# Performance work log

Measured on AMD Instinct MI355X. Metric: run time of the kernel, lower is better.

## Reference

```python
import jax, jax.numpy as jnp
import numpy as np

PRIOR = 0.2
TEMP = 1.0
THRESHOLD = 0.5
B, L, D, H = 8, 4096, 768, 512


def setup_inputs() -> dict:
    key = jax.random.key(0)
    k1, k2, k3, k4 = jax.random.split(key, 4)
    hidden = jax.random.normal(k1, (B, L, D), jnp.float32)
    # MLP params: Linear(D,H) -> ReLU -> Linear(H,1)
    W1 = jax.random.normal(k2, (D, H), jnp.float32) / np.sqrt(D).astype(np.float32)
    b1 = jnp.zeros((H,), jnp.float32)
    W2 = jax.random.normal(k3, (H, 1), jnp.float32) / np.sqrt(H).astype(np.float32)
    b2 = jnp.zeros((1,), jnp.float32)
    # pre-sampled uniform noise for the RelaxedBernoulli logistic reparameterization
    noise_u = jax.random.uniform(k4, (B, L), jnp.float32, minval=1e-6, maxval=1.0 - 1e-6)
    return dict(hidden=hidden, W1=W1, b1=b1, W2=W2, b2=b2, noise_u=noise_u)


def reference(hidden, W1, b1, W2, b2, noise_u):
    bs, seq_len, model_dim = hidden.shape
    # boundary MLP -> per-token logits [B, L]
    h = jax.nn.relu(jnp.einsum('bld,dh->blh', hidden, W1) + b1)
    logits = (jnp.einsum('blh,ho->blo', h, W2) + b2)[..., 0]
    # RelaxedBernoulli rsample: sigmoid((logits + logistic_noise) / temp),
    # since logit(sigmoid(logits)) == logits
    logistic_noise = jnp.log(noise_u) - jnp.log1p(-noise_u)
    soft_boundaries = jax.nn.sigmoid((logits + logistic_noise) / TEMP)
    hard_bin = (soft_boundaries > THRESHOLD).astype(soft_boundaries.dtype)
    # straight-through estimator
    hard_boundaries = soft_boundaries + jax.lax.stop_gradient(hard_bin - soft_boundaries)
    # segment id of each token: number of boundaries strictly before it
    # (boundary token is the last element of its segment)
    seg = (jnp.cumsum(hard_bin, axis=1) - hard_bin).astype(jnp.int32)  # [B, L] in [0, L)
    ids = (seg + seq_len * jnp.arange(bs, dtype=jnp.int32)[:, None]).reshape(-1)
    flat = hidden.reshape(bs * seq_len, model_dim)
    seg_sum = jax.ops.segment_sum(flat, ids, num_segments=bs * seq_len)
    seg_cnt = jax.ops.segment_sum(jnp.ones((bs * seq_len,), hidden.dtype), ids,
                                  num_segments=bs * seq_len)
    # mean pooling per segment; unused segment slots stay zero (padded to L segments,
    # equivalent to the torch [S,B,D]->transpose output up to zero padding)
    pooled = (seg_sum / jnp.maximum(seg_cnt, 1.0)[:, None]).reshape(bs, seq_len, model_dim)
    # hinge loss on boundary rate: penalize |rate - (prior+0.05)| beyond margin 0.05
    ratio = jnp.mean(hard_boundaries)
    loss = jax.nn.relu(jnp.abs(ratio - (PRIOR + 0.05)) - 0.05)
    num_boundaries = jnp.sum(hard_bin)
    total_positions = jnp.asarray(bs * seq_len, jnp.float32)
    return pooled, loss, num_boundaries, total_positions
```

## Files before the change

### kernel.cpp

```cpp
#include <hip/hip_runtime.h>
#include <math.h>

typedef __attribute__((ext_vector_type(8))) short short8;
typedef __attribute__((ext_vector_type(4))) float float4v;
typedef unsigned int uint;

#define BATCH 8
#define SEQ   4096
#define DIM   768
#define HID   512
#define M_TOK (BATCH * SEQ)

static __device__ __forceinline__ short f2bf_rne(float x) {
    unsigned int u = __float_as_uint(x);
    unsigned int r = (u + 0x7FFFu + ((u >> 16) & 1u)) >> 16;
    return (short)r;
}
static __device__ __forceinline__ uint pack_bf2(float a, float b) {
    return __builtin_amdgcn_perm(__float_as_uint(b), __float_as_uint(a), 0x07060302u);
}

__global__ __launch_bounds__(256) void prep_kernel(const float* __restrict__ W1,
                                                   short* __restrict__ W1T) {
    int idx = blockIdx.x * 256 + threadIdx.x;
    if (idx < DIM * HID) {
        int k = idx / HID, n = idx % HID;
        W1T[n * DIM + k] = f2bf_rne(W1[idx]);
    }
}

__global__ __launch_bounds__(256) void mlp_kernel(const float* __restrict__ A,
                                                  const short* __restrict__ BT,
                                                  const float* __restrict__ b1,
                                                  const float* __restrict__ W2,
                                                  float* __restrict__ partial) {
    __shared__ short As[128 * 40];
    __shared__ short Bs[128 * 40];

    const int id  = blockIdx.x;
    const int m_t = (id & 7) + ((id >> 5) << 3);
    const int n_t = (id >> 3) & 3;
    const int m0 = m_t << 7, n0 = n_t << 7;

    const int tid  = threadIdx.x;
    const int srow = tid >> 1;
    const int shalf = tid & 1;
    const int wave = tid >> 6, lane = tid & 63;
    const int quad = lane >> 4, r = lane & 15;
    const int waveM = (wave & 1) << 6, waveN = (wave >> 1) << 6;

    float4v acc[4][4] = {};

    const float* aRow = A + (size_t)(m0 + srow) * DIM + shalf * 16;
    const short* bRow = BT + (size_t)(n0 + srow) * DIM + shalf * 16;

    const int lw = srow * 40 + shalf * 16;
    const int la = (waveM + r) * 40 + quad * 8;
    const int lb = (waveN + r) * 40 + quad * 8;

    float4v fA[2][4];
    short8  fB[2][2];
#pragma unroll
    for (int i = 0; i < 4; i++) fA[0][i] = *(const float4v*)(aRow + i * 4);
    fB[0][0] = *(const short8*)(bRow);
    fB[0][1] = *(const short8*)(bRow + 8);

#pragma unroll
    for (int it = 0; it < 24; ++it) {
        const int cur = it & 1;
        if (it + 1 < 24) {
            const float* ap = aRow + (it + 1) * 32;
            const short* bp = bRow + (it + 1) * 32;
#pragma unroll
            for (int i = 0; i < 4; i++) fA[cur ^ 1][i] = *(const float4v*)(ap + i * 4);
            fB[cur ^ 1][0] = *(const short8*)(bp);
            fB[cur ^ 1][1] = *(const short8*)(bp + 8);
        }
        uint pk[8];
#pragma unroll
        for (int i = 0; i < 4; i++) {
            pk[2 * i]     = pack_bf2(fA[cur][i][0], fA[cur][i][1]);
            pk[2 * i + 1] = pack_bf2(fA[cur][i][2], fA[cur][i][3]);
        }
        __syncthreads();
        *(short8*)(&As[lw])     = *(short8*)&pk[0];
        *(short8*)(&As[lw + 8]) = *(short8*)&pk[4];
        *(short8*)(&Bs[lw])     = fB[cur][0];
        *(short8*)(&Bs[lw + 8]) = fB[cur][1];
        __syncthreads();

        short8 af[4], bf[4];
#pragma unroll
        for (int i = 0; i < 4; i++) {
            af[i] = *(const short8*)(&As[la + i * 16 * 40]);
            bf[i] = *(const short8*)(&Bs[lb + i * 16 * 40]);
        }
#pragma unroll
        for (int mi = 0; mi < 4; mi++)
#pragma unroll
            for (int ni = 0; ni < 4; ni++)
                acc[mi][ni] = __builtin_amdgcn_mfma_f32_16x16x32_bf16(
                    af[mi], bf[ni], acc[mi][ni], 0, 0, 0);
    }

    float w2v[4], b1v[4];
#pragma unroll
    for (int ni = 0; ni < 4; ni++) {
        int gc = n0 + waveN + ni * 16 + r;
        w2v[ni] = W2[gc];
        b1v[ni] = b1[gc];
    }
    const int buf = n_t * 2 + (waveN >> 6);
#pragma unroll
    for (int mi = 0; mi < 4; mi++) {
#pragma unroll
        for (int v = 0; v < 4; v++) {
            float p = 0.f;
#pragma unroll
            for (int ni = 0; ni < 4; ni++) {
                float h = acc[mi][ni][v] + b1v[ni];
                h = h > 0.f ? h : 0.f;
                p += h * w2v[ni];
            }
#pragma unroll
            for (int off = 1; off < 16; off <<= 1) p += __shfl_xor(p, off, 64);
            if (r == 0) {
                int gr = m0 + waveM + mi * 16 + quad * 4 + v;
                partial[(size_t)buf * M_TOK + gr] = p;
            }
        }
    }
}

__global__ __launch_bounds__(1024) void boundary_kernel(const float* __restrict__ partial,
                                                        const float* __restrict__ b2p,
                                                        const float* __restrict__ noise,
                                                        int* __restrict__ starts,
                                                        int* __restrict__ nseg,
                                                        int* __restrict__ nbcount) {
    const int b = blockIdx.x, tid = threadIdx.x;
    const int base = tid * 4;
    const float b2 = b2p[0];
    int h[4], c = 0;
#pragma unroll
    for (int j = 0; j < 4; j++) {
        int l = base + j;
        float u = noise[b * SEQ + l];
        float nz = logf(u) - log1pf(-u);
        float lg = b2 + nz;
#pragma unroll
        for (int q = 0; q < 8; q++) lg += partial[(size_t)q * M_TOK + b * SEQ + l];
        h[j] = (lg > 0.f) ? 1 : 0;
        c += h[j];
    }
    const int lane = tid & 63, wid = tid >> 6;
    int inc = c;
    for (int off = 1; off < 64; off <<= 1) {
        int t = __shfl_up(inc, off, 64);
        if (lane >= off) inc += t;
    }
    __shared__ int wtot[16], woff[16], extra[2];
    if (lane == 63) wtot[wid] = inc;
    if (tid == 1023) extra[0] = h[3];
    __syncthreads();
    if (tid == 0) {
        int s = 0;
        for (int i = 0; i < 16; i++) { woff[i] = s; s += wtot[i]; }
        extra[1] = s;
    }
    __syncthreads();
    int run = (inc - c) + woff[wid];
#pragma unroll
    for (int j = 0; j < 4; j++) {
        int l = base + j;
        if (h[j]) {
            run++;
            if (l < SEQ - 1) starts[b * (SEQ + 1) + run] = l + 1;
        }
    }
    if (tid == 0) {
        int total = extra[1];
        int ns = total + (extra[0] ? 0 : 1);
        starts[b * (SEQ + 1)] = 0;
        starts[b * (SEQ + 1) + ns] = SEQ;
        nseg[b] = ns;
        nbcount[b] = total;
    }
}

__global__ __launch_bounds__(256) void pool_kernel(const float* __restrict__ hidden,
                                                   const int* __restrict__ starts,
                                                   const int* __restrict__ nseg,
                                                   float* __restrict__ out) {
    const int wid = threadIdx.x >> 6, lane = threadIdx.x & 63;
    const int s = blockIdx.x * 4 + wid, b = blockIdx.y;
    float* orow = out + (size_t)(b * SEQ + s) * DIM;
    const int ns = nseg[b];
    if (s >= ns) {
        float4v z = {0.f, 0.f, 0.f, 0.f};
        *(float4v*)(orow + lane * 4)         = z;
        *(float4v*)(orow + (lane + 64) * 4)  = z;
        *(float4v*)(orow + (lane + 128) * 4) = z;
        return;
    }
    const int st = starts[b * (SEQ + 1) + s];
    const int en = starts[b * (SEQ + 1) + s + 1];
    float4v a0 = {0.f, 0.f, 0.f, 0.f}, a1 = a0, a2 = a0;
    const float* hbase = hidden + (size_t)(b * SEQ) * DIM;
    for (int row = st; row < en; row++) {
        const float* hr = hbase + (size_t)row * DIM;
        a0 += *(const float4v*)(hr + lane * 4);
        a1 += *(const float4v*)(hr + (lane + 64) * 4);
        a2 += *(const float4v*)(hr + (lane + 128) * 4);
    }
    const float invc = 1.f / (float)(en - st);
    a0 *= invc; a1 *= invc; a2 *= invc;
    *(float4v*)(orow + lane * 4)         = a0;
    *(float4v*)(orow + (lane + 64) * 4)  = a1;
    *(float4v*)(orow + (lane + 128) * 4) = a2;
}

__global__ void finalize_kernel(const int* __restrict__ nbcount, float* __restrict__ tail) {
    int nb = 0;
    for (int i = 0; i < BATCH; i++) nb += nbcount[i];
    float ratio = (float)nb / (float)M_TOK;
    float d = fabsf(ratio - 0.25f) - 0.05f;
    tail[0] = d > 0.f ? d : 0.f;
    tail[1] = (float)nb;
    tail[2] = (float)M_TOK;
}

extern "C" void kernel_launch(void* const* d_in, const int* in_sizes, int n_in,
                              void* d_out, int out_size, void* d_ws, size_t ws_size,
                              hipStream_t stream) {
    const float* hidden = (const float*)d_in[0];
    const float* W1     = (const float*)d_in[1];
    const float* b1     = (const float*)d_in[2];
    const float* W2     = (const float*)d_in[3];
    const float* b2     = (const float*)d_in[4];
    const float* noise  = (const float*)d_in[5];

    char* ws = (char*)d_ws;
    short* W1T     = (short*)(ws);
    float* partial = (float*)(ws + 786432);
    int*   starts  = (int*)(ws + 786432 + 1048576);
    int*   nseg    = (int*)(ws + 786432 + 1048576 + 131104);
    int*   nbcount = nseg + 8;
    float* out     = (float*)d_out;

    prep_kernel<<<1536, 256, 0, stream>>>(W1, W1T);
    mlp_kernel<<<1024, 256, 0, stream>>>(hidden, W1T, b1, W2, partial);
    boundary_kernel<<<BATCH, 1024, 0, stream>>>(partial, b2, noise, starts, nseg, nbcount);
    pool_kernel<<<dim3(SEQ / 4, BATCH), 256, 0, stream>>>(hidden, starts, nseg, out);
    finalize_kernel<<<1, 1, 0, stream>>>(nbcount, out + (size_t)M_TOK * DIM);
}
```

Baseline: 256.2 us.

## Load A fragments directly into registers and split boundary scan into parallel kernels

The MLP GEMM now has each wave load its own 16 rows of fp32 activations straight from global memory into MFMA fragment registers, converting them to bf16 there, so activations no longer pass through LDS. Only W1 is staged in shared memory, the tile becomes 64x128 with a 64-wide K step, and the grid doubles to 2048 blocks. The single-block-per-batch boundary scan is replaced by a 64-block ballot kernel that writes bitmasks and popcounts, followed by a 64-block kernel that scatters segment starts. The aim is to cut LDS traffic and barriers in the GEMM and to parallelise the serial scan, at the cost of uncoalesced A loads and an extra kernel launch.

```diff
diff --git a/kernel.cpp b/kernel.cpp
--- a/kernel.cpp
+++ b/kernel.cpp
@@ -19,6 +19,7 @@
 static __device__ __forceinline__ uint pack_bf2(float a, float b) {
     return __builtin_amdgcn_perm(__float_as_uint(b), __float_as_uint(a), 0x07060302u);
 }
+union FragU { uint u[4]; short8 s; };
 
 __global__ __launch_bounds__(256) void prep_kernel(const float* __restrict__ W1,
                                                    short* __restrict__ W1T) {
@@ -34,157 +35,154 @@
                                                   const float* __restrict__ b1,
                                                   const float* __restrict__ W2,
                                                   float* __restrict__ partial) {
-    __shared__ short As[128 * 40];
-    __shared__ short Bs[128 * 40];
-
-    const int id  = blockIdx.x;
-    const int m_t = (id & 7) + ((id >> 5) << 3);
-    const int n_t = (id >> 3) & 3;
-    const int m0 = m_t << 7, n0 = n_t << 7;
-
-    const int tid  = threadIdx.x;
-    const int srow = tid >> 1;
-    const int shalf = tid & 1;
-    const int wave = tid >> 6, lane = tid & 63;
+    __shared__ short Bs[2 * 128 * 40];
+
+    const int id   = blockIdx.x;
+    const int row8 = id & 7;
+    const int n_g  = (id >> 3) & 3;
+    const int m_t  = (id >> 5) * 8 + row8;
+    const int m0 = m_t * 64, n0 = n_g * 128;
+
+    const int tid = threadIdx.x, wave = tid >> 6, lane = tid & 63;
     const int quad = lane >> 4, r = lane & 15;
-    const int waveM = (wave & 1) << 6, waveN = (wave >> 1) << 6;
-
-    float4v acc[4][4] = {};
-
-    const float* aRow = A + (size_t)(m0 + srow) * DIM + shalf * 16;
-    const short* bRow = BT + (size_t)(n0 + srow) * DIM + shalf * 16;
-
-    const int lw = srow * 40 + shalf * 16;
-    const int la = (waveM + r) * 40 + quad * 8;
-    const int lb = (waveN + r) * 40 + quad * 8;
+
+    const float* aRow = A + (size_t)(m0 + wave * 16 + r) * DIM + quad * 8;
+    const short* bRow = BT + (size_t)(n0 + (tid >> 1)) * DIM + (tid & 1) * 32;
+    const int bwr = (tid & 1) * 5120 + (tid >> 1) * 40;
 
     float4v fA[2][4];
-    short8  fB[2][2];
-#pragma unroll
-    for (int i = 0; i < 4; i++) fA[0][i] = *(const float4v*)(aRow + i * 4);
-    fB[0][0] = *(const short8*)(bRow);
-    fB[0][1] = *(const short8*)(bRow + 8);
-
-#pragma unroll
-    for (int it = 0; it < 24; ++it) {
+    short8  fB[2][4];
+#pragma unroll
+    for (int i = 0; i < 4; i++) fB[0][i] = *(const short8*)(bRow + i * 8);
+    fA[0][0] = *(const float4v*)(aRow + 0);
+    fA[0][1] = *(const float4v*)(aRow + 4);
+    fA[0][2] = *(const float4v*)(aRow + 32);
+    fA[0][3] = *(const float4v*)(aRow + 36);
+
+    float4v acc[8] = {};
+
+#pragma unroll
+    for (int it = 0; it < 12; ++it) {
         const int cur = it & 1;
-        if (it + 1 < 24) {
-            const float* ap = aRow + (it + 1) * 32;
-            const short* bp = bRow + (it + 1) * 32;
-#pragma unroll
-            for (int i = 0; i < 4; i++) fA[cur ^ 1][i] = *(const float4v*)(ap + i * 4);
-            fB[cur ^ 1][0] = *(const short8*)(bp);
-            fB[cur ^ 1][1] = *(const short8*)(bp + 8);
-        }
-        uint pk[8];
-#pragma unroll
-        for (int i = 0; i < 4; i++) {
-            pk[2 * i]     = pack_bf2(fA[cur][i][0], fA[cur][i][1]);
-            pk[2 * i + 1] = pack_bf2(fA[cur][i][2], fA[cur][i][3]);
+        if (it < 11) {
+            const float* ap = aRow + (it + 1) * 64;
+            fA[cur ^ 1][0] = *(const float4v*)(ap + 0);
+            fA[cur ^ 1][1] = *(const float4v*)(ap + 4);
+            fA[cur ^ 1][2] = *(const float4v*)(ap + 32);
+            fA[cur ^ 1][3] = *(const float4v*)(ap + 36);
+            const short* bp = bRow + (it + 1) * 64;
+#pragma unroll
+            for (int i = 0; i < 4; i++) fB[cur ^ 1][i] = *(const short8*)(bp + i * 8);
         }
         __syncthreads();
-        *(short8*)(&As[lw])     = *(short8*)&pk[0];
-        *(short8*)(&As[lw + 8]) = *(short8*)&pk[4];
-        *(short8*)(&Bs[lw])     = fB[cur][0];
-        *(short8*)(&Bs[lw + 8]) = fB[cur][1];
+#pragma unroll
+        for (int i = 0; i < 4; i++) *(short8*)(&Bs[bwr + i * 8]) = fB[cur][i];
         __syncthreads();
 
-        short8 af[4], bf[4];
-#pragma unroll
-        for (int i = 0; i < 4; i++) {
-            af[i] = *(const short8*)(&As[la + i * 16 * 40]);
-            bf[i] = *(const short8*)(&Bs[lb + i * 16 * 40]);
-        }
-#pragma unroll
-        for (int mi = 0; mi < 4; mi++)
-#pragma unroll
-            for (int ni = 0; ni < 4; ni++)
-                acc[mi][ni] = __builtin_amdgcn_mfma_f32_16x16x32_bf16(
-                    af[mi], bf[ni], acc[mi][ni], 0, 0, 0);
-    }
-
-    float w2v[4], b1v[4];
-#pragma unroll
-    for (int ni = 0; ni < 4; ni++) {
-        int gc = n0 + waveN + ni * 16 + r;
-        w2v[ni] = W2[gc];
-        b1v[ni] = b1[gc];
-    }
-    const int buf = n_t * 2 + (waveN >> 6);
-#pragma unroll
-    for (int mi = 0; mi < 4; mi++) {
-#pragma unroll
-        for (int v = 0; v < 4; v++) {
-            float p = 0.f;
-#pragma unroll
-            for (int ni = 0; ni < 4; ni++) {
-                float h = acc[mi][ni][v] + b1v[ni];
-                h = h > 0.f ? h : 0.f;
-                p += h * w2v[ni];
+#pragma unroll
+        for (int ks = 0; ks < 2; ks++) {
+            FragU af;
+            af.u[0] = pack_bf2(fA[cur][ks * 2][0], fA[cur][ks * 2][1]);
+            af.u[1] = pack_bf2(fA[cur][ks * 2][2], fA[cur][ks * 2][3]);
+            af.u[2] = pack_bf2(fA[cur][ks * 2 + 1][0], fA[cur][ks * 2 + 1][1]);
+            af.u[3] = pack_bf2(fA[cur][ks * 2 + 1][2], fA[cur][ks * 2 + 1][3]);
+#pragma unroll
+            for (int j = 0; j < 8; j++) {
+                short8 bf = *(const short8*)(&Bs[ks * 5120 + (j * 16 + r) * 40 + quad * 8]);
+                acc[j] = __builtin_amdgcn_mfma_f32_16x16x32_bf16(af.s, bf, acc[j], 0, 0, 0);
             }
-#pragma unroll
-            for (int off = 1; off < 16; off <<= 1) p += __shfl_xor(p, off, 64);
-            if (r == 0) {
-                int gr = m0 + waveM + mi * 16 + quad * 4 + v;
-                partial[(size_t)buf * M_TOK + gr] = p;
-            }
-        }
-    }
-}
-
-__global__ __launch_bounds__(1024) void boundary_kernel(const float* __restrict__ partial,
-                                                        const float* __restrict__ b2p,
-                                                        const float* __restrict__ noise,
-                                                        int* __restrict__ starts,
-                                                        int* __restrict__ nseg,
-                                                        int* __restrict__ nbcount) {
-    const int b = blockIdx.x, tid = threadIdx.x;
-    const int base = tid * 4;
+        }
+    }
+
+    float b1v[8], w2v[8];
+#pragma unroll
+    for (int j = 0; j < 8; j++) {
+        int gc = n0 + j * 16 + r;
+        b1v[j] = b1[gc];
+        w2v[j] = W2[gc];
+    }
+#pragma unroll
+    for (int v = 0; v < 4; v++) {
+        float p = 0.f;
+#pragma unroll
+        for (int j = 0; j < 8; j++) {
+            float h = acc[j][v] + b1v[j];
+            h = h > 0.f ? h : 0.f;
+            p += h * w2v[j];
+        }
+#pragma unroll
+        for (int off = 1; off < 16; off <<= 1) p += __shfl_xor(p, off, 64);
+        if (r == 0)
+            partial[(size_t)n_g * M_TOK + m0 + wave * 16 + quad * 4 + v] = p;
+    }
+}
+
+__global__ __launch_bounds__(256) void bits_kernel(const float* __restrict__ partial,
+                                                   const float* __restrict__ b2p,
+                                                   const float* __restrict__ noise,
+                                                   unsigned long long* __restrict__ bits,
+                                                   int* __restrict__ counts) {
+    const int blk = blockIdx.x;
+    const int tid = threadIdx.x, wid = tid >> 6, lane = tid & 63;
     const float b2 = b2p[0];
-    int h[4], c = 0;
-#pragma unroll
-    for (int j = 0; j < 4; j++) {
-        int l = base + j;
-        float u = noise[b * SEQ + l];
-        float nz = logf(u) - log1pf(-u);
-        float lg = b2 + nz;
-#pragma unroll
-        for (int q = 0; q < 8; q++) lg += partial[(size_t)q * M_TOK + b * SEQ + l];
-        h[j] = (lg > 0.f) ? 1 : 0;
-        c += h[j];
-    }
-    const int lane = tid & 63, wid = tid >> 6;
-    int inc = c;
-    for (int off = 1; off < 64; off <<= 1) {
-        int t = __shfl_up(inc, off, 64);
-        if (lane >= off) inc += t;
-    }
-    __shared__ int wtot[16], woff[16], extra[2];
-    if (lane == 63) wtot[wid] = inc;
-    if (tid == 1023) extra[0] = h[3];
+    __shared__ int pc[8];
+    const int base = blk * 512;
+#pragma unroll
+    for (int h = 0; h < 2; h++) {
+        int l = base + h * 256 + tid;
+        float u = noise[l];
+        float lg = b2 + logf(u) - log1pf(-u);
+#pragma unroll
+        for (int q = 0; q < 4; q++) lg += partial[(size_t)q * M_TOK + l];
+        unsigned long long bal = __ballot(lg > 0.f);
+        if (lane == 0) {
+            bits[blk * 8 + h * 4 + wid] = bal;
+            pc[h * 4 + wid] = __popcll(bal);
+        }
+    }
     __syncthreads();
     if (tid == 0) {
         int s = 0;
-        for (int i = 0; i < 16; i++) { woff[i] = s; s += wtot[i]; }
-        extra[1] = s;
-    }
+        for (int i = 0; i < 8; i++) s += pc[i];
+        counts[blk] = s;
+    }
+}
+
+__global__ __launch_bounds__(256) void starts_kernel(const unsigned long long* __restrict__ bits,
+                                                     const int* __restrict__ counts,
+                                                     int* __restrict__ starts,
+                                                     int* __restrict__ nseg) {
+    const int blk = blockIdx.x, b = blk >> 3, s8 = blk & 7;
+    const int tid = threadIdx.x, wid = tid >> 6, lane = tid & 63;
+    __shared__ int cs[9];
+    __shared__ unsigned long long ms[8];
+    if (tid == 0) {
+        int s = 0;
+        for (int i = 0; i < 8; i++) { cs[i] = s; s += counts[b * 8 + i]; }
+        cs[8] = s;
+    }
+    if (tid < 8) ms[tid] = bits[blk * 8 + tid];
     __syncthreads();
-    int run = (inc - c) + woff[wid];
-#pragma unroll
-    for (int j = 0; j < 4; j++) {
-        int l = base + j;
-        if (h[j]) {
-            run++;
-            if (l < SEQ - 1) starts[b * (SEQ + 1) + run] = l + 1;
-        }
-    }
-    if (tid == 0) {
-        int total = extra[1];
-        int ns = total + (extra[0] ? 0 : 1);
+    const int blockoff = cs[s8];
+#pragma unroll
+    for (int h = 0; h < 2; h++) {
+        int j = h * 4 + wid;
+        unsigned long long mask = ms[j];
+        if (!((mask >> lane) & 1ULL)) continue;
+        int pre = blockoff;
+        for (int i = 0; i < j; i++) pre += __popcll(ms[i]);
+        pre += __popcll(lane ? (mask & (~0ULL >> (64 - lane))) : 0ULL);
+        int lb = s8 * 512 + j * 64 + lane;
+        int run = pre + 1;
+        if (lb < SEQ - 1) starts[b * (SEQ + 1) + run] = lb + 1;
+    }
+    if (s8 == 7 && tid == 0) {
+        int nb = cs[8];
+        int lastbit = (int)(ms[7] >> 63) & 1;
+        int ns = nb + (lastbit ? 0 : 1);
         starts[b * (SEQ + 1)] = 0;
         starts[b * (SEQ + 1) + ns] = SEQ;
         nseg[b] = ns;
-        nbcount[b] = total;
     }
 }
 
@@ -220,9 +218,9 @@
     *(float4v*)(orow + (lane + 128) * 4) = a2;
 }
 
-__global__ void finalize_kernel(const int* __restrict__ nbcount, float* __restrict__ tail) {
+__global__ void finalize_kernel(const int* __restrict__ counts, float* __restrict__ tail) {
     int nb = 0;
-    for (int i = 0; i < BATCH; i++) nb += nbcount[i];
+    for (int i = 0; i < 64; i++) nb += counts[i];
     float ratio = (float)nb / (float)M_TOK;
     float d = fabsf(ratio - 0.25f) - 0.05f;
     tail[0] = d > 0.f ? d : 0.f;
@@ -243,14 +241,16 @@
     char* ws = (char*)d_ws;
     short* W1T     = (short*)(ws);
     float* partial = (float*)(ws + 786432);
-    int*   starts  = (int*)(ws + 786432 + 1048576);
-    int*   nseg    = (int*)(ws + 786432 + 1048576 + 131104);
-    int*   nbcount = nseg + 8;
+    int*   starts  = (int*)(ws + 1310720);
+    unsigned long long* bits = (unsigned long long*)(ws + 1441824);
+    int*   counts  = (int*)(ws + 1445920);
+    int*   nseg    = (int*)(ws + 1446176);
     float* out     = (float*)d_out;
 
     prep_kernel<<<1536, 256, 0, stream>>>(W1, W1T);
-    mlp_kernel<<<1024, 256, 0, stream>>>(hidden, W1T, b1, W2, partial);
-    boundary_kernel<<<BATCH, 1024, 0, stream>>>(partial, b2, noise, starts, nseg, nbcount);
+    mlp_kernel<<<2048, 256, 0, stream>>>(hidden, W1T, b1, W2, partial);
+    bits_kernel<<<64, 256, 0, stream>>>(partial, b2, noise, bits, counts);
+    starts_kernel<<<64, 256, 0, stream>>>(bits, counts, starts, nseg);
     pool_kernel<<<dim3(SEQ / 4, BATCH), 256, 0, stream>>>(hidden, starts, nseg, out);
-    finalize_kernel<<<1, 1, 0, stream>>>(nbcount, out + (size_t)M_TOK * DIM);
-}
+    finalize_kernel<<<1, 1, 0, stream>>>(counts, out + (size_t)M_TOK * DIM);
+}
```

Result: no change. 258.7 us (+1.0%).

## Retile MLP GEMM to full-N 64-row blocks with register-resident W1 fragments

Applied to the files above, without the earlier changes.

The MLP kernel now assigns each block 64 token rows and all 512 hidden columns, so each fp32 hidden row is read and converted to bf16 only once instead of four times. W1 fragments are loaded straight from global memory into registers with double buffering, which drops B-tile shared-memory staging. The A tile is double-buffered in LDS with one barrier per 64-wide K step. Partial logits shrink from 8 to 4 buffers, but accumulator registers double (32 float4 per lane), which may lower occupancy, and B loads from global/L2 grow.

```diff
diff --git a/kernel.cpp b/kernel.cpp
--- a/kernel.cpp
+++ b/kernel.cpp
@@ -19,6 +19,7 @@
 static __device__ __forceinline__ uint pack_bf2(float a, float b) {
     return __builtin_amdgcn_perm(__float_as_uint(b), __float_as_uint(a), 0x07060302u);
 }
+union FragU { uint u[4]; short8 s; };
 
 __global__ __launch_bounds__(256) void prep_kernel(const float* __restrict__ W1,
                                                    short* __restrict__ W1T) {
@@ -34,102 +35,101 @@
                                                   const float* __restrict__ b1,
                                                   const float* __restrict__ W2,
                                                   float* __restrict__ partial) {
-    __shared__ short As[128 * 40];
-    __shared__ short Bs[128 * 40];
-
-    const int id  = blockIdx.x;
-    const int m_t = (id & 7) + ((id >> 5) << 3);
-    const int n_t = (id >> 3) & 3;
-    const int m0 = m_t << 7, n0 = n_t << 7;
-
-    const int tid  = threadIdx.x;
-    const int srow = tid >> 1;
-    const int shalf = tid & 1;
+    __shared__ short As[2][64 * 72];
+
+    const int m0 = blockIdx.x * 64;
+    const int tid = threadIdx.x;
     const int wave = tid >> 6, lane = tid & 63;
     const int quad = lane >> 4, r = lane & 15;
-    const int waveM = (wave & 1) << 6, waveN = (wave >> 1) << 6;
-
-    float4v acc[4][4] = {};
-
-    const float* aRow = A + (size_t)(m0 + srow) * DIM + shalf * 16;
-    const short* bRow = BT + (size_t)(n0 + srow) * DIM + shalf * 16;
-
-    const int lw = srow * 40 + shalf * 16;
-    const int la = (waveM + r) * 40 + quad * 8;
-    const int lb = (waveN + r) * 40 + quad * 8;
-
-    float4v fA[2][4];
-    short8  fB[2][2];
-#pragma unroll
-    for (int i = 0; i < 4; i++) fA[0][i] = *(const float4v*)(aRow + i * 4);
-    fB[0][0] = *(const short8*)(bRow);
-    fB[0][1] = *(const short8*)(bRow + 8);
-
-#pragma unroll
-    for (int it = 0; it < 24; ++it) {
-        const int cur = it & 1;
-        if (it + 1 < 24) {
-            const float* ap = aRow + (it + 1) * 32;
-            const short* bp = bRow + (it + 1) * 32;
-#pragma unroll
-            for (int i = 0; i < 4; i++) fA[cur ^ 1][i] = *(const float4v*)(ap + i * 4);
-            fB[cur ^ 1][0] = *(const short8*)(bp);
-            fB[cur ^ 1][1] = *(const short8*)(bp + 8);
-        }
+    const int srow = tid >> 2, scol = (tid & 3) * 16;
+    const float* aPtr = A + (size_t)(m0 + srow) * DIM + scol;
+    const int lw = srow * 72 + scol;
+    const short* bPtr = BT + (size_t)(wave * 128 + r) * DIM + quad * 8;
+
+    float4v s[4];
+    short8  bfr[2][8];
+#pragma unroll
+    for (int i = 0; i < 4; i++) s[i] = *(const float4v*)(aPtr + i * 4);
+#pragma unroll
+    for (int j = 0; j < 8; j++) bfr[0][j] = *(const short8*)(bPtr + j * 16 * DIM);
+    {
         uint pk[8];
 #pragma unroll
         for (int i = 0; i < 4; i++) {
-            pk[2 * i]     = pack_bf2(fA[cur][i][0], fA[cur][i][1]);
-            pk[2 * i + 1] = pack_bf2(fA[cur][i][2], fA[cur][i][3]);
+            pk[2 * i]     = pack_bf2(s[i][0], s[i][1]);
+            pk[2 * i + 1] = pack_bf2(s[i][2], s[i][3]);
+        }
+        *(short8*)(&As[0][lw])     = *(short8*)&pk[0];
+        *(short8*)(&As[0][lw + 8]) = *(short8*)&pk[4];
+    }
+    float4v acc[4][8] = {};
+    __syncthreads();
+
+    int ks = 0;
+#pragma unroll
+    for (int p = 0; p < 12; ++p) {
+        const int cur = p & 1;
+        if (p < 11) {
+            const float* ap = aPtr + (p + 1) * 64;
+#pragma unroll
+            for (int i = 0; i < 4; i++) s[i] = *(const float4v*)(ap + i * 4);
+        }
+#pragma unroll
+        for (int h = 0; h < 2; ++h, ++ks) {
+            const int bb = ks & 1;
+            if (ks < 23) {
+                const short* bp = bPtr + (ks + 1) * 32;
+#pragma unroll
+                for (int j = 0; j < 8; j++)
+                    bfr[bb ^ 1][j] = *(const short8*)(bp + j * 16 * DIM);
+            }
+            FragU af[4];
+#pragma unroll
+            for (int mf = 0; mf < 4; mf++)
+                af[mf].s = *(const short8*)(&As[cur][(mf * 16 + r) * 72 + h * 32 + quad * 8]);
+#pragma unroll
+            for (int mf = 0; mf < 4; mf++)
+#pragma unroll
+                for (int j = 0; j < 8; j++)
+                    acc[mf][j] = __builtin_amdgcn_mfma_f32_16x16x32_bf16(
+                        af[mf].s, bfr[bb][j], acc[mf][j], 0, 0, 0);
+        }
+        if (p < 11) {
+            uint pk[8];
+#pragma unroll
+            for (int i = 0; i < 4; i++) {
+                pk[2 * i]     = pack_bf2(s[i][0], s[i][1]);
+                pk[2 * i + 1] = pack_bf2(s[i][2], s[i][3]);
+            }
+            *(short8*)(&As[cur ^ 1][lw])     = *(short8*)&pk[0];
+            *(short8*)(&As[cur ^ 1][lw + 8]) = *(short8*)&pk[4];
         }
         __syncthreads();
-        *(short8*)(&As[lw])     = *(short8*)&pk[0];
-        *(short8*)(&As[lw + 8]) = *(short8*)&pk[4];
-        *(short8*)(&Bs[lw])     = fB[cur][0];
-        *(short8*)(&Bs[lw + 8]) = fB[cur][1];
-        __syncthreads();
-
-        short8 af[4], bf[4];
-#pragma unroll
-        for (int i = 0; i < 4; i++) {
-            af[i] = *(const short8*)(&As[la + i * 16 * 40]);
-            bf[i] = *(const short8*)(&Bs[lb + i * 16 * 40]);
-        }
-#pragma unroll
-        for (int mi = 0; mi < 4; mi++)
-#pragma unroll
-            for (int ni = 0; ni < 4; ni++)
-                acc[mi][ni] = __builtin_amdgcn_mfma_f32_16x16x32_bf16(
-                    af[mi], bf[ni], acc[mi][ni], 0, 0, 0);
-    }
-
-    float w2v[4], b1v[4];
-#pragma unroll
-    for (int ni = 0; ni < 4; ni++) {
-        int gc = n0 + waveN + ni * 16 + r;
-        w2v[ni] = W2[gc];
-        b1v[ni] = b1[gc];
-    }
-    const int buf = n_t * 2 + (waveN >> 6);
-#pragma unroll
-    for (int mi = 0; mi < 4; mi++) {
+    }
+
+    float b1v[8], w2v[8];
+#pragma unroll
+    for (int j = 0; j < 8; j++) {
+        int gc = wave * 128 + j * 16 + r;
+        b1v[j] = b1[gc];
+        w2v[j] = W2[gc];
+    }
+#pragma unroll
+    for (int mf = 0; mf < 4; mf++)
 #pragma unroll
         for (int v = 0; v < 4; v++) {
-            float p = 0.f;
-#pragma unroll
-            for (int ni = 0; ni < 4; ni++) {
-                float h = acc[mi][ni][v] + b1v[ni];
-                h = h > 0.f ? h : 0.f;
-                p += h * w2v[ni];
+            float pp = 0.f;
+#pragma unroll
+            for (int j = 0; j < 8; j++) {
+                float hh = acc[mf][j][v] + b1v[j];
+                hh = hh > 0.f ? hh : 0.f;
+                pp += hh * w2v[j];
             }
 #pragma unroll
-            for (int off = 1; off < 16; off <<= 1) p += __shfl_xor(p, off, 64);
-            if (r == 0) {
-                int gr = m0 + waveM + mi * 16 + quad * 4 + v;
-                partial[(size_t)buf * M_TOK + gr] = p;
-            }
-        }
-    }
+            for (int off = 1; off < 16; off <<= 1) pp += __shfl_xor(pp, off, 64);
+            if (r == 0)
+                partial[(size_t)wave * M_TOK + m0 + mf * 16 + quad * 4 + v] = pp;
+        }
 }
 
 __global__ __launch_bounds__(1024) void boundary_kernel(const float* __restrict__ partial,
@@ -149,7 +149,7 @@
         float nz = logf(u) - log1pf(-u);
         float lg = b2 + nz;
 #pragma unroll
-        for (int q = 0; q < 8; q++) lg += partial[(size_t)q * M_TOK + b * SEQ + l];
+        for (int q = 0; q < 4; q++) lg += partial[(size_t)q * M_TOK + b * SEQ + l];
         h[j] = (lg > 0.f) ? 1 : 0;
         c += h[j];
     }
@@ -243,13 +243,13 @@
     char* ws = (char*)d_ws;
     short* W1T     = (short*)(ws);
     float* partial = (float*)(ws + 786432);
-    int*   starts  = (int*)(ws + 786432 + 1048576);
-    int*   nseg    = (int*)(ws + 786432 + 1048576 + 131104);
+    int*   starts  = (int*)(ws + 1310720);
+    int*   nseg    = (int*)(ws + 1441824);
     int*   nbcount = nseg + 8;
     float* out     = (float*)d_out;
 
     prep_kernel<<<1536, 256, 0, stream>>>(W1, W1T);
-    mlp_kernel<<<1024, 256, 0, stream>>>(hidden, W1T, b1, W2, partial);
+    mlp_kernel<<<512, 256, 0, stream>>>(hidden, W1T, b1, W2, partial);
     boundary_kernel<<<BATCH, 1024, 0, stream>>>(partial, b2, noise, starts, nseg, nbcount);
     pool_kernel<<<dim3(SEQ / 4, BATCH), 256, 0, stream>>>(hidden, starts, nseg, out);
     finalize_kernel<<<1, 1, 0, stream>>>(nbcount, out + (size_t)M_TOK * DIM);
```

After: 263.5 us. +2.8%, slower.
